# Optimization experiments

Measured on AMD Instinct MI355X. Metric: run time of the kernel, lower is better.

The kernel has to match this reference:

```python
import jax, jax.numpy as jnp
import numpy as np

VOCAB, EMB, H = 50000, 300, 64  # fgian_config: embed_dim=300, hidden_dim=64
POL = 3


def _lstm(x, lens, Wih, Whh, b):
    """Masked unidirectional LSTM (PyTorch gate order i,f,g,o).
    x: [B,T,D]; outputs zero past each sequence's length (packed-LSTM semantics)."""
    B, T, _ = x.shape
    Hh = Whh.shape[1]
    xs = jnp.einsum('btd,gd->btg', x, Wih) + b  # precompute input projection [B,T,4H]

    def step(carry, inp):
        h, c = carry
        xproj, t = inp
        g = xproj + h @ Whh.T
        i, f, gg, o = jnp.split(g, 4, axis=-1)
        i = jax.nn.sigmoid(i); f = jax.nn.sigmoid(f)
        gg = jnp.tanh(gg); o = jax.nn.sigmoid(o)
        c_new = f * c + i * gg
        h_new = o * jnp.tanh(c_new)
        m = (t < lens)[:, None]
        return (jnp.where(m, h_new, h), jnp.where(m, c_new, c)), jnp.where(m, h_new, 0.0)

    h0 = jnp.zeros((B, Hh), x.dtype)
    _, out = jax.lax.scan(step, (h0, h0), (xs.transpose(1, 0, 2), jnp.arange(T)))
    return out.transpose(1, 0, 2)


def _bilstm(x, lens, Wih_f, Whh_f, b_f, Wih_b, Whh_b, b_b):
    B, T, _ = x.shape
    t = jnp.arange(T)
    fwd = _lstm(x, lens, Wih_f, Whh_f, b_f)
    # reverse each sequence within its valid length, run fwd scan, reverse back
    ridx = jnp.clip(lens[:, None] - 1 - t[None, :], 0)  # [B,T]
    x_rev = jnp.take_along_axis(x, ridx[..., None], axis=1)
    bwd_rev = _lstm(x_rev, lens, Wih_b, Whh_b, b_b)
    bwd = jnp.take_along_axis(bwd_rev, ridx[..., None], axis=1)
    bwd = jnp.where((t[None, :] < lens[:, None])[..., None], bwd, 0.0)
    return jnp.concatenate([fwd, bwd], axis=-1)  # [B,T,2H]


def setup_inputs() -> dict:
    key = jax.random.key(0)
    ks = jax.random.split(key, 20)
    s = 0.1
    d = {
        'body_idx': jax.random.randint(ks[0], (128, 512), 0, VOCAB),
        'pun_idx': jax.random.randint(ks[1], (128, 256), 0, VOCAB),
        'emb': jax.random.normal(ks[2], (VOCAB, EMB), jnp.float32) * s,
        'w_u': jax.random.normal(ks[15], (6 * H,), jnp.float32) * s,
        'Wd': jax.random.normal(ks[16], (POL, 4 * H), jnp.float32) * s,
        'bd': jnp.zeros((POL,), jnp.float32),
    }
    names = ['bWih_f', 'bWhh_f', 'bb_f', 'bWih_b', 'bWhh_b', 'bb_b',
             'pWih_f', 'pWhh_f', 'pb_f', 'pWih_b', 'pWhh_b', 'pb_b']
    shapes = [(4 * H, EMB), (4 * H, H), (4 * H,)] * 4
    for i, (n, sh) in enumerate(zip(names, shapes)):
        d[n] = jax.random.normal(ks[3 + i], sh, jnp.float32) * s
    return d


def reference(body_idx, pun_idx, emb,
              bWih_f, bWhh_f, bb_f, bWih_b, bWhh_b, bb_b,
              pWih_f, pWhh_f, pb_f, pWih_b, pWhh_b, pb_b,
              w_u, Wd, bd):
    body_len = jnp.sum(body_idx != 0, axis=1)
    pun_len = jnp.sum(pun_idx != 0, axis=1)
    body_M = _bilstm(emb[body_idx], body_len, bWih_f, bWhh_f, bb_f, bWih_b, bWhh_b, bb_b)  # [B,T,2H]
    pun_M = _bilstm(emb[pun_idx], pun_len, pWih_f, pWhh_f, pb_f, pWih_b, pWhh_b, pb_b)     # [B,P,2H]

    # alignment[b,i,j] = [body_i, pun_j, body_i*pun_j] . w_u  -> fully vectorized
    w1, w2, w3 = jnp.split(w_u, 3)
    align = (jnp.einsum('btd,d->bt', body_M, w1)[:, :, None]
             + jnp.einsum('bpd,d->bp', pun_M, w2)[:, None, :]
             + jnp.einsum('btd,bpd->btp', body_M * w3, pun_M))  # [B,T,P]

    att_b = jax.nn.softmax(align.max(axis=2), axis=1)  # [B,T]
    f_pun2body = jnp.einsum('btd,bt->bd', body_M, att_b)
    att_p = jax.nn.softmax(align.max(axis=1), axis=1)  # [B,P]
    f_body2pun = jnp.einsum('bp,bpd->bd', att_p, pun_M)

    feat = jnp.concatenate([f_pun2body, f_body2pun], axis=1)  # [B,4H]
    return feat @ Wd.T + bd
```

## Files before the change

kernel.cpp:

```cpp
#include <hip/hip_runtime.h>


#define B 128
#define TBODY 512
#define TPUN 256
#define EMB 300
#define EMBP 320
#define VOCAB 50000
#define HID 64
#define G4 256
#define NG 512
#define DM 128

typedef __attribute__((ext_vector_type(8))) short bf16x8;
typedef __attribute__((ext_vector_type(4))) float floatx4;
typedef unsigned short u16;

#define OFF_XPB   0u
#define OFF_XPP   134217728u
#define OFF_BODYM 201326592u
#define OFF_PUNM  234881024u
#define OFF_SMALL 251658240u
#define OFF_ABODY (OFF_XPB + 0u)
#define OFF_APUN  (OFF_XPB + 262144u)
#define OFF_MT    (OFF_XPB + 393216u)
#define OFF_MP    (OFF_XPB + 655360u)
#define OFF_COLP  (OFF_XPB + 786432u)
#define OFF_EMBB  OFF_BODYM
#define OFF_WCB   OFF_PUNM
#define OFF_WCP   (OFF_PUNM + 327680u)
#define OFF_BIASB (OFF_PUNM + 655360u)
#define OFF_BIASP (OFF_PUNM + 657408u)
#define OFF_LENS  OFF_SMALL
#define OFF_FEAT  (OFF_SMALL + 1024u)

__device__ inline u16 f2bf(float v) {
    unsigned int u = __float_as_uint(v);
    unsigned int r = (u + 0x7FFFu + ((u >> 16) & 1u)) >> 16;
    return (u16)r;
}

__device__ inline void gload_lds16(const void* g, void* l) {
    __builtin_amdgcn_global_load_lds(
        (const __attribute__((address_space(1))) unsigned int*)g,
        (__attribute__((address_space(3))) unsigned int*)l, 16, 0, 0);
}

#define RL(v, k) __int_as_float(__builtin_amdgcn_readlane(__float_as_int(v), k))
#define SWZ(v, pat) __int_as_float(__builtin_amdgcn_ds_swizzle(__float_as_int(v), pat))

__global__ __launch_bounds__(256) void k_lens(const int* __restrict__ bidx,
                                              const int* __restrict__ pidx,
                                              int* __restrict__ lens) {
    int j = blockIdx.x, tid = threadIdx.x;
    const int* src; int n;
    if (j < B) { src = bidx + (size_t)j * TBODY; n = TBODY; }
    else       { src = pidx + (size_t)(j - B) * TPUN; n = TPUN; }
    int c = 0;
    for (int t = tid; t < n; t += 256) c += (src[t] != 0) ? 1 : 0;
    for (int o = 32; o; o >>= 1) c += __shfl_xor(c, o, 64);
    __shared__ int red[4];
    if ((tid & 63) == 0) red[tid >> 6] = c;
    __syncthreads();
    if (tid == 0) lens[j] = red[0] + red[1] + red[2] + red[3];
}

__global__ __launch_bounds__(256) void k_prep_emb(const float* __restrict__ emb,
                                                  u16* __restrict__ embb) {
    int e = blockIdx.x * 256 + threadIdx.x;
    int row = e / EMBP, d = e - row * EMBP;
    float v = (d < EMB) ? emb[(size_t)row * EMB + d] : 0.f;
    embb[e] = f2bf(v);
}

__global__ __launch_bounds__(256) void k_prep_w(
    const float* __restrict__ bWih_f, const float* __restrict__ bWih_b,
    const float* __restrict__ bb_f, const float* __restrict__ bb_b,
    const float* __restrict__ pWih_f, const float* __restrict__ pWih_b,
    const float* __restrict__ pb_f, const float* __restrict__ pb_b,
    u16* __restrict__ Wcb, u16* __restrict__ Wcp,
    float* __restrict__ biasb, float* __restrict__ biasp) {
    int e = blockIdx.x * 256 + threadIdx.x;
    const int WSZ = NG * EMBP;
    if (e < WSZ) {
        int g = e / EMBP, d = e - g * EMBP;
        float v = 0.f;
        if (d < EMB) v = (g < G4) ? bWih_f[g * EMB + d] : bWih_b[(g - G4) * EMB + d];
        Wcb[e] = f2bf(v);
    } else if (e < 2 * WSZ) {
        int ee = e - WSZ;
        int g = ee / EMBP, d = ee - g * EMBP;
        float v = 0.f;
        if (d < EMB) v = (g < G4) ? pWih_f[g * EMB + d] : pWih_b[(g - G4) * EMB + d];
        Wcp[ee] = f2bf(v);
    } else if (e < 2 * WSZ + NG) {
        int g = e - 2 * WSZ;
        biasb[g] = (g < G4) ? bb_f[g] : bb_b[g - G4];
    } else if (e < 2 * WSZ + 2 * NG) {
        int g = e - 2 * WSZ - NG;
        biasp[g] = (g < G4) ? pb_f[g] : pb_b[g - G4];
    }
}

__global__ __launch_bounds__(256) void k_gemm(const int* __restrict__ idx,
                                              const u16* __restrict__ embb,
                                              const u16* __restrict__ Wc,
                                              const float* __restrict__ biasc,
                                              float* __restrict__ out) {
    __shared__ u16 As[128 * 32];
    __shared__ u16 Bs[128 * 32];
    int tid = threadIdx.x, wave = tid >> 6, lane = tid & 63;
    int m0 = blockIdx.x * 128, g0 = blockIdx.y * 128;

    const u16* agp[2]; const u16* bgp[2];
    u16* asd[2]; u16* bsd[2];
#pragma unroll
    for (int j = 0; j < 2; j++) {
        int rbase = wave * 32 + j * 16;
        int r = rbase + (lane >> 2);
        int clog = (lane & 3) ^ (r & 3);
        int arow = idx[m0 + r];
        agp[j] = embb + (size_t)arow * EMBP + clog * 8;
        bgp[j] = Wc + (size_t)(g0 + r) * EMBP + clog * 8;
        asd[j] = As + rbase * 32;
        bsd[j] = Bs + rbase * 32;
    }

    int l15 = lane & 15, quad = lane >> 4;
    int mt0 = (wave >> 1) * 4, nt0 = (wave & 1) * 4;
    const u16* ard[4]; const u16* brd[4];
#pragma unroll
    for (int a = 0; a < 4; a++) {
        int r = (mt0 + a) * 16 + l15;
        ard[a] = As + r * 32 + ((quad ^ (r & 3)) * 8);
        int n = (nt0 + a) * 16 + l15;
        brd[a] = Bs + n * 32 + ((quad ^ (n & 3)) * 8);
    }

    floatx4 acc[4][4];
#pragma unroll
    for (int a = 0; a < 4; a++)
#pragma unroll
        for (int c = 0; c < 4; c++) acc[a][c] = (floatx4){0.f, 0.f, 0.f, 0.f};

    for (int k0 = 0; k0 < EMBP; k0 += 32) {
#pragma unroll
        for (int j = 0; j < 2; j++) {
            gload_lds16(agp[j] + k0, asd[j]);
            gload_lds16(bgp[j] + k0, bsd[j]);
        }
        __syncthreads();
        bf16x8 af[4], bfr[4];
#pragma unroll
        for (int a = 0; a < 4; a++) { af[a] = *(const bf16x8*)ard[a]; bfr[a] = *(const bf16x8*)brd[a]; }
#pragma unroll
        for (int a = 0; a < 4; a++)
#pragma unroll
            for (int c = 0; c < 4; c++)
                acc[a][c] = __builtin_amdgcn_mfma_f32_16x16x32_bf16(af[a], bfr[c], acc[a][c], 0, 0, 0);
        __syncthreads();
    }

#pragma unroll
    for (int c = 0; c < 4; c++) {
        int gcol = g0 + (nt0 + c) * 16 + l15;
        float bv = biasc[gcol];
#pragma unroll
        for (int a = 0; a < 4; a++) {
            int row0 = m0 + (mt0 + a) * 16 + quad * 4;
#pragma unroll
            for (int rg = 0; rg < 4; rg++)
                out[(size_t)(row0 + rg) * NG + gcol] = acc[a][c][rg] + bv;
        }
    }
}

#define DECLW(j) float Wk##j##0 = vw[4*j], Wk##j##1 = vw[4*j+1], \
                       Wk##j##2 = vw[4*j+2], Wk##j##3 = vw[4*j+3];
#define STEP4(j) \
    a0 = fmaf(RL(hq.x, j), Wk##j##0, a0); \
    a1 = fmaf(RL(hq.y, j), Wk##j##1, a1); \
    a2 = fmaf(RL(hq.z, j), Wk##j##2, a2); \
    a3 = fmaf(RL(hq.w, j), Wk##j##3, a3);

__global__ __launch_bounds__(256, 2) void k_scan(
    const float* __restrict__ xpB, const float* __restrict__ xpP,
    float* __restrict__ bodyM, float* __restrict__ punM,
    const int* __restrict__ lens,
    const float* __restrict__ bWhh_f, const float* __restrict__ bWhh_b,
    const float* __restrict__ pWhh_f, const float* __restrict__ pWhh_b) {
    int task = blockIdx.x, tid = threadIdx.x;
    int isPun = task >> 8;
    int sub = task & 255;
    int b = sub & 127, dir = sub >> 7;
    int T = isPun ? TPUN : TBODY;
    int len = lens[(isPun ? B : 0) + b];
    int w = tid >> 6, l = tid & 63;
    int g = l & 3, q = l >> 2;
    int u = w * 16 + q;
    const float* xp = (isPun ? xpP : xpB) + (size_t)b * T * NG + dir * G4;
    float* outp = (isPun ? punM : bodyM) + (size_t)b * T * DM + dir * HID;
    const float* Whh = isPun ? (dir ? pWhh_b : pWhh_f) : (dir ? bWhh_b : bWhh_f);

    const volatile float* vw = Whh + (size_t)(g * 64 + u) * 64;
    DECLW(0)  DECLW(1)  DECLW(2)  DECLW(3)
    DECLW(4)  DECLW(5)  DECLW(6)  DECLW(7)
    DECLW(8)  DECLW(9)  DECLW(10) DECLW(11)
    DECLW(12) DECLW(13) DECLW(14) DECLW(15)

    __shared__ __align__(16) float hbuf[2][64];
    if (tid < 64) hbuf[0][tid] = 0.f;
    __syncthreads();
    if (len <= 0) return;

    const float* xg = xp + g * 64 + u;
    float c = 0.f;
    float x_cur = xg[(size_t)(dir ? (len - 1) : 0) * NG];
    for (int s = 0; s < len; ++s) {
        int p = dir ? (len - 1 - s) : s;
        float xv = x_cur;
        int pn = dir ? (len - 2 - s) : (s + 1);
        pn = min(max(pn, 0), T - 1);
        x_cur = xg[(size_t)pn * NG];

        float4 hq = *(const float4*)(&hbuf[s & 1][(l & 15) * 4]);
        float a0 = xv, a1 = 0.f, a2 = 0.f, a3 = 0.f;
        STEP4(0)  STEP4(1)  STEP4(2)  STEP4(3)
        STEP4(4)  STEP4(5)  STEP4(6)  STEP4(7)
        STEP4(8)  STEP4(9)  STEP4(10) STEP4(11)
        STEP4(12) STEP4(13) STEP4(14) STEP4(15)
        float pre = (a0 + a1) + (a2 + a3);
        bool isg = (g == 2);
        float t_in = isg ? (2.f * pre) : (-pre);
        float e = __expf(t_in);
        float r = __builtin_amdgcn_rcpf(1.f + e);
        float val = isg ? fmaf(-2.f, r, 1.f) : r;
        float vi = SWZ(val, 0x8000);
        float vf = SWZ(val, 0x8055);
        float vg = SWZ(val, 0x80AA);
        float vo = SWZ(val, 0x80FF);
        c = fmaf(vf, c, vi * vg);
        float th = fmaf(-2.f, __builtin_amdgcn_rcpf(1.f + __expf(2.f * c)), 1.f);
        float h = vo * th;
        if (g == 0) {
            hbuf[(s & 1) ^ 1][u] = h;
            outp[(size_t)p * DM + u] = h;
        }
        __syncthreads();
    }
}

__global__ __launch_bounds__(256) void k_rowdot(const float* __restrict__ bodyM,
                                                const float* __restrict__ punM,
                                                const float* __restrict__ w_u,
                                                float* __restrict__ a_body,
                                                float* __restrict__ a_pun) {
    int wid = (blockIdx.x * 256 + threadIdx.x) >> 6;
    int lane = threadIdx.x & 63;
    const int NB = B * TBODY;
    const float* src; const float* wv; float* dst;
    if (wid < NB) { src = bodyM + (size_t)wid * DM; wv = w_u; dst = a_body + wid; }
    else { src = punM + (size_t)(wid - NB) * DM; wv = w_u + DM; dst = a_pun + (wid - NB); }
    float2 v = ((const float2*)src)[lane];
    float2 w = ((const float2*)wv)[lane];
    float s = v.x * w.x + v.y * w.y;
    for (int o = 32; o; o >>= 1) s += __shfl_xor(s, o, 64);
    if (lane == 0) *dst = s;
}

__global__ __launch_bounds__(256) void k_align(
    const float* __restrict__ bodyM, const float* __restrict__ punM,
    const float* __restrict__ a_body, const float* __restrict__ a_pun,
    const float* __restrict__ w_u,
    float* __restrict__ m_t, float* __restrict__ colpart) {
    __shared__ float bw[64 * 132];
    __shared__ float pu[64 * 129];
    __shared__ float colred[64 * 16];
    int tid = threadIdx.x;
    int tt = blockIdx.x, b = blockIdx.y;
    int t0 = tt * 64;
    int ti = tid >> 4, pi = tid & 15;
    const float* w3 = w_u + 2 * DM;
    const float* bsrc = bodyM + ((size_t)b * TBODY + t0) * DM;
#pragma unroll
    for (int j = 0; j < 8; j++) {
        int e = tid + 256 * j;
        int i = e >> 5, c4 = e & 31;
        float4 v = *(const float4*)(bsrc + i * DM + c4 * 4);
        float4 wv = *(const float4*)(w3 + c4 * 4);
        v.x *= wv.x; v.y *= wv.y; v.z *= wv.z; v.w *= wv.w;
        *(float4*)(bw + i * 132 + c4 * 4) = v;
    }
    float aB[4];
#pragma unroll
    for (int a = 0; a < 4; a++) aB[a] = a_body[(size_t)b * TBODY + t0 + ti * 4 + a];
    float mrun[4] = {-1e30f, -1e30f, -1e30f, -1e30f};
    for (int pc = 0; pc < 4; pc++) {
        __syncthreads();
        const float* psrc = punM + ((size_t)b * TPUN + pc * 64) * DM;
#pragma unroll
        for (int j = 0; j < 8; j++) {
            int e = tid + 256 * j;
            int i = e >> 5, c4 = e & 31;
            float4 v = *(const float4*)(psrc + i * DM + c4 * 4);
            pu[i * 129 + c4 * 4 + 0] = v.x;
            pu[i * 129 + c4 * 4 + 1] = v.y;
            pu[i * 129 + c4 * 4 + 2] = v.z;
            pu[i * 129 + c4 * 4 + 3] = v.w;
        }
        __syncthreads();
        float aP[4];
#pragma unroll
        for (int c = 0; c < 4; c++) aP[c] = a_pun[(size_t)b * TPUN + pc * 64 + pi * 4 + c];
        float C[4][4];
#pragma unroll
        for (int a = 0; a < 4; a++)
#pragma unroll
            for (int c = 0; c < 4; c++) C[a][c] = 0.f;
        for (int d4 = 0; d4 < 32; d4++) {
            float4 bq[4];
#pragma unroll
            for (int a = 0; a < 4; a++) bq[a] = *(const float4*)(bw + (ti * 4 + a) * 132 + d4 * 4);
#pragma unroll
            for (int dd = 0; dd < 4; dd++) {
                float pv[4];
#pragma unroll
                for (int c = 0; c < 4; c++) pv[c] = pu[(pi * 4 + c) * 129 + d4 * 4 + dd];
#pragma unroll
                for (int a = 0; a < 4; a++) {
                    float bvv = (dd == 0) ? bq[a].x : (dd == 1) ? bq[a].y : (dd == 2) ? bq[a].z : bq[a].w;
#pragma unroll
                    for (int c = 0; c < 4; c++) C[a][c] += bvv * pv[c];
                }
            }
        }
        float colv[4] = {-1e30f, -1e30f, -1e30f, -1e30f};
#pragma unroll
        for (int a = 0; a < 4; a++) {
            float rm = -1e30f;
#pragma unroll
            for (int c = 0; c < 4; c++) {
                float valv = C[a][c] + aB[a] + aP[c];
                rm = fmaxf(rm, valv);
                colv[c] = fmaxf(colv[c], valv);
            }
#pragma unroll
            for (int o = 1; o < 16; o <<= 1) rm = fmaxf(rm, __shfl_xor(rm, o, 64));
            mrun[a] = fmaxf(mrun[a], rm);
        }
#pragma unroll
        for (int c = 0; c < 4; c++) colred[(pi * 4 + c) * 16 + ti] = colv[c];
        __syncthreads();
        if (tid < 64) {
            float m = -1e30f;
#pragma unroll
            for (int k = 0; k < 16; k++) m = fmaxf(m, colred[tid * 16 + k]);
            colpart[((size_t)b * 8 + tt) * TPUN + pc * 64 + tid] = m;
        }
    }
    if (pi == 0) {
#pragma unroll
        for (int a = 0; a < 4; a++) m_t[(size_t)b * TBODY + t0 + ti * 4 + a] = mrun[a];
    }
}

__global__ __launch_bounds__(256) void k_colmax(const float* __restrict__ colpart,
                                                float* __restrict__ m_p) {
    int b = blockIdx.x, p = threadIdx.x;
    float m = -1e30f;
    for (int tt = 0; tt < 8; tt++) m = fmaxf(m, colpart[((size_t)b * 8 + tt) * TPUN + p]);
    m_p[(size_t)b * TPUN + p] = m;
}

__global__ __launch_bounds__(256) void k_feat(const float* __restrict__ bodyM,
                                              const float* __restrict__ punM,
                                              const float* __restrict__ m_t,
                                              const float* __restrict__ m_p,
                                              float* __restrict__ feat) {
    int bidx = blockIdx.x;
    int b = bidx & (B - 1), which = bidx >> 7;
    int n = which ? TPUN : TBODY;
    const float* sc = which ? (m_p + (size_t)b * TPUN) : (m_t + (size_t)b * TBODY);
    const float* src = which ? (punM + (size_t)b * TPUN * DM) : (bodyM + (size_t)b * TBODY * DM);
    float* dst = feat + (size_t)b * 256 + which * DM;
    int tid = threadIdx.x;
    __shared__ float e_lds[TBODY];
    __shared__ float red[8];
    __shared__ float red2[256];
    float mx = -1e30f;
    for (int t = tid; t < n; t += 256) mx = fmaxf(mx, sc[t]);
    for (int o = 32; o; o >>= 1) mx = fmaxf(mx, __shfl_xor(mx, o, 64));
    if ((tid & 63) == 0) red[tid >> 6] = mx;
    __syncthreads();
    mx = fmaxf(fmaxf(red[0], red[1]), fmaxf(red[2], red[3]));
    float se = 0.f;
    for (int t = tid; t < n; t += 256) {
        float ev = __expf(sc[t] - mx);
        e_lds[t] = ev;
        se += ev;
    }
    for (int o = 32; o; o >>= 1) se += __shfl_xor(se, o, 64);
    if ((tid & 63) == 0) red[4 + (tid >> 6)] = se;
    __syncthreads();
    se = red[4] + red[5] + red[6] + red[7];
    float inv = 1.f / se;
    int d = tid & 127, half = tid >> 7;
    float acc = 0.f;
    for (int t = half; t < n; t += 2) acc += e_lds[t] * src[(size_t)t * DM + d];
    red2[tid] = acc;
    __syncthreads();
    if (tid < DM) dst[tid] = (red2[tid] + red2[tid + 128]) * inv;
}

__global__ __launch_bounds__(256) void k_out(const float* __restrict__ feat,
                                             const float* __restrict__ Wd,
                                             const float* __restrict__ bd,
                                             float* __restrict__ outp) {
    int b = blockIdx.x, tid = threadIdx.x;
    float v = feat[(size_t)b * 256 + tid];
    __shared__ float red[12];
#pragma unroll
    for (int pol = 0; pol < 3; pol++) {
        float s = v * Wd[pol * 256 + tid];
        for (int o = 32; o; o >>= 1) s += __shfl_xor(s, o, 64);
        if ((tid & 63) == 0) red[pol * 4 + (tid >> 6)] = s;
    }
    __syncthreads();
    if (tid < 3) outp[b * 3 + tid] = red[tid * 4] + red[tid * 4 + 1] + red[tid * 4 + 2] + red[tid * 4 + 3] + bd[tid];
}

extern "C" void kernel_launch(void* const* d_in, const int* in_sizes, int n_in,
                              void* d_out, int out_size, void* d_ws, size_t ws_size,
                              hipStream_t stream) {
    const int* body_idx = (const int*)d_in[0];
    const int* pun_idx  = (const int*)d_in[1];
    const float* emb    = (const float*)d_in[2];
    const float* w_u    = (const float*)d_in[3];
    const float* Wd     = (const float*)d_in[4];
    const float* bd     = (const float*)d_in[5];
    const float* bWih_f = (const float*)d_in[6];
    const float* bWhh_f = (const float*)d_in[7];
    const float* bb_f   = (const float*)d_in[8];
    const float* bWih_b = (const float*)d_in[9];
    const float* bWhh_b = (const float*)d_in[10];
    const float* bb_b   = (const float*)d_in[11];
    const float* pWih_f = (const float*)d_in[12];
    const float* pWhh_f = (const float*)d_in[13];
    const float* pb_f   = (const float*)d_in[14];
    const float* pWih_b = (const float*)d_in[15];
    const float* pWhh_b = (const float*)d_in[16];
    const float* pb_b   = (const float*)d_in[17];

    char* ws = (char*)d_ws;
    float* xpB   = (float*)(ws + OFF_XPB);
    float* xpP   = (float*)(ws + OFF_XPP);
    float* bodyM = (float*)(ws + OFF_BODYM);
    float* punM  = (float*)(ws + OFF_PUNM);
    u16* embb    = (u16*)(ws + OFF_EMBB);
    u16* Wcb     = (u16*)(ws + OFF_WCB);
    u16* Wcp     = (u16*)(ws + OFF_WCP);
    float* biasb = (float*)(ws + OFF_BIASB);
    float* biasp = (float*)(ws + OFF_BIASP);
    int* lens    = (int*)(ws + OFF_LENS);
    float* a_body = (float*)(ws + OFF_ABODY);
    float* a_pun  = (float*)(ws + OFF_APUN);
    float* m_t    = (float*)(ws + OFF_MT);
    float* m_p    = (float*)(ws + OFF_MP);
    float* colpart = (float*)(ws + OFF_COLP);
    float* feat   = (float*)(ws + OFF_FEAT);
    float* outp   = (float*)d_out;

    k_lens<<<dim3(256), dim3(256), 0, stream>>>(body_idx, pun_idx, lens);
    k_prep_emb<<<dim3(62500), dim3(256), 0, stream>>>(emb, embb);
    k_prep_w<<<dim3(1284), dim3(256), 0, stream>>>(bWih_f, bWih_b, bb_f, bb_b,
                                                   pWih_f, pWih_b, pb_f, pb_b,
                                                   Wcb, Wcp, biasb, biasp);
    k_gemm<<<dim3(512, 4), dim3(256), 0, stream>>>(body_idx, embb, Wcb, biasb, xpB);
    k_gemm<<<dim3(256, 4), dim3(256), 0, stream>>>(pun_idx, embb, Wcp, biasp, xpP);
    hipMemsetAsync(ws + OFF_BODYM, 0, (size_t)(33554432u + 16777216u), stream);
    k_scan<<<dim3(512), dim3(256), 0, stream>>>(xpB, xpP, bodyM, punM, lens,
                                                bWhh_f, bWhh_b, pWhh_f, pWhh_b);
    k_rowdot<<<dim3(24576), dim3(256), 0, stream>>>(bodyM, punM, w_u, a_body, a_pun);
    k_align<<<dim3(8, 128), dim3(256), 0, stream>>>(bodyM, punM, a_body, a_pun, w_u, m_t, colpart);
    k_colmax<<<dim3(128), dim3(256), 0, stream>>>(colpart, m_p);
    k_feat<<<dim3(256), dim3(256), 0, stream>>>(bodyM, punM, m_t, m_p, feat);
    k_out<<<dim3(128), dim3(256), 0, stream>>>(feat, Wd, bd, outp);
}
```

Measured before the change: 716.0 us.

## Split LSTM recurrent dot product across four wave groups with LDS reduction

The scan kernel grows from 256 to 1024 threads per block. Each of four wave groups now handles a 16-wide slice of the hidden dimension, reading h as broadcast float4 values from LDS instead of using 64 serial readlanes. The partial sums go into a shared buffer and are combined after an extra barrier. This shortens the per-step critical path on the serial recurrence. In exchange it adds one more block-wide barrier per timestep across 16 waves, and every wave group computes the gate nonlinearities redundantly.

```diff
diff --git a/kernel.cpp b/kernel.cpp
--- a/kernel.cpp
+++ b/kernel.cpp
@@ -46,7 +46,6 @@
         (__attribute__((address_space(3))) unsigned int*)l, 16, 0, 0);
 }
 
-#define RL(v, k) __int_as_float(__builtin_amdgcn_readlane(__float_as_int(v), k))
 #define SWZ(v, pat) __int_as_float(__builtin_amdgcn_ds_swizzle(__float_as_int(v), pat))
 
 __global__ __launch_bounds__(256) void k_lens(const int* __restrict__ bidx,
@@ -175,15 +174,7 @@
     }
 }
 
-#define DECLW(j) float Wk##j##0 = vw[4*j], Wk##j##1 = vw[4*j+1], \
-                       Wk##j##2 = vw[4*j+2], Wk##j##3 = vw[4*j+3];
-#define STEP4(j) \
-    a0 = fmaf(RL(hq.x, j), Wk##j##0, a0); \
-    a1 = fmaf(RL(hq.y, j), Wk##j##1, a1); \
-    a2 = fmaf(RL(hq.z, j), Wk##j##2, a2); \
-    a3 = fmaf(RL(hq.w, j), Wk##j##3, a3);
-
-__global__ __launch_bounds__(256, 2) void k_scan(
+__global__ __launch_bounds__(1024, 2) void k_scan(
     const float* __restrict__ xpB, const float* __restrict__ xpP,
     float* __restrict__ bodyM, float* __restrict__ punM,
     const int* __restrict__ lens,
@@ -195,27 +186,28 @@
     int b = sub & 127, dir = sub >> 7;
     int T = isPun ? TPUN : TBODY;
     int len = lens[(isPun ? B : 0) + b];
-    int w = tid >> 6, l = tid & 63;
+    int wave = tid >> 6, l = tid & 63;
+    int wg = wave >> 2, w_in = wave & 3;
     int g = l & 3, q = l >> 2;
-    int u = w * 16 + q;
+    int u = w_in * 16 + q;
+    int row = g * 64 + u;
     const float* xp = (isPun ? xpP : xpB) + (size_t)b * T * NG + dir * G4;
     float* outp = (isPun ? punM : bodyM) + (size_t)b * T * DM + dir * HID;
     const float* Whh = isPun ? (dir ? pWhh_b : pWhh_f) : (dir ? bWhh_b : bWhh_f);
 
-    const volatile float* vw = Whh + (size_t)(g * 64 + u) * 64;
-    DECLW(0)  DECLW(1)  DECLW(2)  DECLW(3)
-    DECLW(4)  DECLW(5)  DECLW(6)  DECLW(7)
-    DECLW(8)  DECLW(9)  DECLW(10) DECLW(11)
-    DECLW(12) DECLW(13) DECLW(14) DECLW(15)
+    const float4* wr = (const float4*)(Whh + (size_t)row * 64 + wg * 16);
+    float4 w0 = wr[0], w1 = wr[1], w2 = wr[2], w3 = wr[3];
 
     __shared__ __align__(16) float hbuf[2][64];
+    __shared__ __align__(16) float part[256 * 4];
     if (tid < 64) hbuf[0][tid] = 0.f;
     __syncthreads();
     if (len <= 0) return;
 
-    const float* xg = xp + g * 64 + u;
+    const float* xg = xp + row;
     float c = 0.f;
     float x_cur = xg[(size_t)(dir ? (len - 1) : 0) * NG];
+    bool writer = (g == 0) && (wg == 0);
     for (int s = 0; s < len; ++s) {
         int p = dir ? (len - 1 - s) : s;
         float xv = x_cur;
@@ -223,13 +215,19 @@
         pn = min(max(pn, 0), T - 1);
         x_cur = xg[(size_t)pn * NG];
 
-        float4 hq = *(const float4*)(&hbuf[s & 1][(l & 15) * 4]);
-        float a0 = xv, a1 = 0.f, a2 = 0.f, a3 = 0.f;
-        STEP4(0)  STEP4(1)  STEP4(2)  STEP4(3)
-        STEP4(4)  STEP4(5)  STEP4(6)  STEP4(7)
-        STEP4(8)  STEP4(9)  STEP4(10) STEP4(11)
-        STEP4(12) STEP4(13) STEP4(14) STEP4(15)
-        float pre = (a0 + a1) + (a2 + a3);
+        const float4* hb = (const float4*)(&hbuf[s & 1][wg * 16]);
+        float4 h0 = hb[0], h1 = hb[1], h2 = hb[2], h3 = hb[3];
+        float p0 = h0.x * w0.x, p1 = h0.y * w0.y, p2 = h0.z * w0.z, p3 = h0.w * w0.w;
+        p0 = fmaf(h1.x, w1.x, p0); p1 = fmaf(h1.y, w1.y, p1);
+        p2 = fmaf(h1.z, w1.z, p2); p3 = fmaf(h1.w, w1.w, p3);
+        p0 = fmaf(h2.x, w2.x, p0); p1 = fmaf(h2.y, w2.y, p1);
+        p2 = fmaf(h2.z, w2.z, p2); p3 = fmaf(h2.w, w2.w, p3);
+        p0 = fmaf(h3.x, w3.x, p0); p1 = fmaf(h3.y, w3.y, p1);
+        p2 = fmaf(h3.z, w3.z, p2); p3 = fmaf(h3.w, w3.w, p3);
+        part[row * 4 + wg] = (p0 + p1) + (p2 + p3);
+        __syncthreads();
+        float4 p4 = *(const float4*)(&part[row * 4]);
+        float pre = ((p4.x + p4.y) + (p4.z + p4.w)) + xv;
         bool isg = (g == 2);
         float t_in = isg ? (2.f * pre) : (-pre);
         float e = __expf(t_in);
@@ -237,12 +235,12 @@
         float val = isg ? fmaf(-2.f, r, 1.f) : r;
         float vi = SWZ(val, 0x8000);
         float vf = SWZ(val, 0x8055);
-        float vg = SWZ(val, 0x80AA);
+        float vgg = SWZ(val, 0x80AA);
         float vo = SWZ(val, 0x80FF);
-        c = fmaf(vf, c, vi * vg);
+        c = fmaf(vf, c, vi * vgg);
         float th = fmaf(-2.f, __builtin_amdgcn_rcpf(1.f + __expf(2.f * c)), 1.f);
         float h = vo * th;
-        if (g == 0) {
+        if (writer) {
             hbuf[(s & 1) ^ 1][u] = h;
             outp[(size_t)p * DM + u] = h;
         }
@@ -478,8 +476,8 @@
     k_gemm<<<dim3(512, 4), dim3(256), 0, stream>>>(body_idx, embb, Wcb, biasb, xpB);
     k_gemm<<<dim3(256, 4), dim3(256), 0, stream>>>(pun_idx, embb, Wcp, biasp, xpP);
     hipMemsetAsync(ws + OFF_BODYM, 0, (size_t)(33554432u + 16777216u), stream);
-    k_scan<<<dim3(512), dim3(256), 0, stream>>>(xpB, xpP, bodyM, punM, lens,
-                                                bWhh_f, bWhh_b, pWhh_f, pWhh_b);
+    k_scan<<<dim3(512), dim3(1024), 0, stream>>>(xpB, xpP, bodyM, punM, lens,
+                                                 bWhh_f, bWhh_b, pWhh_f, pWhh_b);
     k_rowdot<<<dim3(24576), dim3(256), 0, stream>>>(bodyM, punM, w_u, a_body, a_pun);
     k_align<<<dim3(8, 128), dim3(256), 0, stream>>>(bodyM, punM, a_body, a_pun, w_u, m_t, colpart);
     k_colmax<<<dim3(128), dim3(256), 0, stream>>>(colpart, m_p);
```

Result: slower. 744.0 us (+3.9%).
